# Kernel optimization log

Hardware: AMD Instinct MI355X
Metric: run time of the kernel (lower is better)

## Reference

```python
import jax, jax.numpy as jnp
import numpy as np

N_EMBD = 2048
N_HEAD = 32
N_GROUPS = 8
HEAD_DIM = N_EMBD // N_HEAD
Q_PER_KV = N_HEAD // N_GROUPS
QKV_DIM = (Q_PER_KV + 2) * N_GROUPS * HEAD_DIM


def apply_rope(x, cos, sin):
    # x: [B, nH, T, hd]; cos/sin: [T, rot//2]
    B, nH, T, hd = x.shape
    rot = min(sin.shape[1] * 2, hd)
    half = rot // 2
    x_rot, x_pass = x[..., :rot], x[..., rot:]
    c = cos[:T, :half][None, None]  # [1,1,T,half]
    s = sin[:T, :half][None, None]
    x1, x2 = x_rot[..., :half], x_rot[..., half:]
    x1_ = x1 * c - x2 * s
    x2_ = x2 * c + x1 * s
    return jnp.concatenate([x1_, x2_, x_pass], axis=-1)


def setup_inputs() -> dict:
    key = jax.random.key(0)
    k1, k2, k3, k4, k5 = jax.random.split(key, 5)
    B, T = 2, 2048
    x = jax.random.normal(k1, (B, T, N_EMBD), dtype=jnp.float32)
    cos = jax.random.uniform(k2, (T, HEAD_DIM // 2), dtype=jnp.float32)
    sin = jax.random.uniform(k3, (T, HEAD_DIM // 2), dtype=jnp.float32)
    attn_w = jax.random.normal(k4, (QKV_DIM, N_EMBD), dtype=jnp.float32) * (1.0 / np.sqrt(N_EMBD))
    proj_w = jax.random.normal(k5, (N_EMBD, N_EMBD), dtype=jnp.float32) * (1.0 / np.sqrt(N_EMBD))
    return {"x": x, "cos": cos, "sin": sin, "attn_w": attn_w, "proj_w": proj_w}


def reference(x, cos, sin, attn_w, proj_w):
    B, T, E = x.shape
    qkv = jnp.einsum('bte,fe->btf', x, attn_w)  # [B,T,QKV_DIM]
    qkv = qkv.reshape(B, T, N_GROUPS, Q_PER_KV + 2, HEAD_DIM)
    q = qkv[:, :, :, :Q_PER_KV].reshape(B, T, N_HEAD, HEAD_DIM)
    k = qkv[:, :, :, Q_PER_KV]      # [B,T,G,hd]
    v = qkv[:, :, :, Q_PER_KV + 1]  # [B,T,G,hd]
    # [B, heads, T, hd] layout; GQA repeat_interleave of K/V to full head count
    q = q.transpose(0, 2, 1, 3)
    k = jnp.repeat(k.transpose(0, 2, 1, 3), Q_PER_KV, axis=1)
    v = jnp.repeat(v.transpose(0, 2, 1, 3), Q_PER_KV, axis=1)
    q = apply_rope(q, cos, sin)
    k = apply_rope(k, cos, sin)
    scale = 1.0 / np.sqrt(HEAD_DIM)
    att = jax.nn.softmax(jnp.einsum('bhqd,bhkd->bhqk', q, k) * scale, axis=-1)
    out = jnp.einsum('bhqk,bhkd->bhqd', att, v)  # [B,nH,T,hd]
    out = out.transpose(0, 2, 1, 3).reshape(B, T, N_HEAD * HEAD_DIM)
    return jnp.einsum('bte,fe->btf', out, proj_w)
```

## Files before the change

kernel.cpp:

```cpp
#include <hip/hip_runtime.h>

typedef unsigned short u16;
typedef unsigned int u32;
typedef __bf16 bf16x8 __attribute__((ext_vector_type(8)));
typedef float f32x4 __attribute__((ext_vector_type(4)));
typedef float f32x16 __attribute__((ext_vector_type(16)));

__device__ __forceinline__ u16 f2bf(float f) {
    u32 u = __builtin_bit_cast(u32, f);
    u32 r = u + 0x7FFFu + ((u >> 16) & 1u);
    return (u16)(r >> 16);
}
__device__ __forceinline__ u32 pack_bf16(float v0, float v1) {
    u32 a = __builtin_bit_cast(u32, v0) + 0x8000u;
    u32 b = __builtin_bit_cast(u32, v1) + 0x8000u;
    return __builtin_amdgcn_perm(b, a, 0x07060302u);
}
__device__ __forceinline__ void gload16(const u16* g, u16* l) {
    __builtin_amdgcn_global_load_lds(
        (const __attribute__((address_space(1))) u32*)g,
        (__attribute__((address_space(3))) u32*)l, 16, 0, 0);
}

#define QSCALE 0.18033688011111793f

__global__ __launch_bounds__(256) void cvt_kernel(const float* __restrict__ in,
                                                  u16* __restrict__ out, int n4) {
    int i = blockIdx.x * 256 + threadIdx.x;
    if (i >= n4) return;
    float4 f = reinterpret_cast<const float4*>(in)[i];
    u32 lo = (u32)f2bf(f.x) | ((u32)f2bf(f.y) << 16);
    u32 hi = (u32)f2bf(f.z) | ((u32)f2bf(f.w) << 16);
    reinterpret_cast<uint2*>(out)[i] = make_uint2(lo, hi);
}

__global__ __launch_bounds__(256) void gemm_qkv(const u16* __restrict__ A,
                                                const u16* __restrict__ Bw,
                                                const float* __restrict__ cosb,
                                                const float* __restrict__ sinb,
                                                u16* __restrict__ Qo,
                                                u16* __restrict__ Ko,
                                                u16* __restrict__ Vt) {
    __shared__ __align__(16) u16 As[2 * 128 * 32];
    __shared__ __align__(16) u16 Bs[2 * 128 * 32];
    const int tid = threadIdx.x;
    const int wave = tid >> 6, lane = tid & 63, quad = lane >> 4, l15 = lane & 15;
    const int wm = wave >> 1, wn = wave & 1;
    const int m0 = blockIdx.x * 128, n0 = blockIdx.y * 128;
    const int K = 2048;
    const int lrow = lane >> 2, lcol = (lane & 3) * 8;
    f32x4 acc[4][4];
#pragma unroll
    for (int a = 0; a < 4; a++)
#pragma unroll
        for (int b = 0; b < 4; b++) acc[a][b] = (f32x4){0.f, 0.f, 0.f, 0.f};
    for (int kk = 0; kk < K; kk += 64) {
        __syncthreads();
#pragma unroll
        for (int p = 0; p < 2; p++)
#pragma unroll
            for (int c = 0; c < 2; c++) {
                const int rA = wave * 32 + c * 16;
                gload16(A  + (size_t)(m0 + rA + lrow) * K + kk + p * 32 + lcol,
                        &As[p * 4096 + rA * 32]);
                gload16(Bw + (size_t)(n0 + rA + lrow) * K + kk + p * 32 + lcol,
                        &Bs[p * 4096 + rA * 32]);
            }
        __syncthreads();
#pragma unroll
        for (int p = 0; p < 2; p++) {
            bf16x8 af[4], bfr[4];
#pragma unroll
            for (int t = 0; t < 4; t++) {
                af[t]  = *reinterpret_cast<const bf16x8*>(
                    &As[p * 4096 + (wm * 64 + t * 16 + l15) * 32 + quad * 8]);
                bfr[t] = *reinterpret_cast<const bf16x8*>(
                    &Bs[p * 4096 + (wn * 64 + t * 16 + l15) * 32 + quad * 8]);
            }
#pragma unroll
            for (int tm = 0; tm < 4; tm++)
#pragma unroll
                for (int tn = 0; tn < 4; tn++)
                    acc[tm][tn] = __builtin_amdgcn_mfma_f32_16x16x32_bf16(af[tm], bfr[tn], acc[tm][tn], 0, 0, 0);
        }
    }
    const int slot_base = n0 + wn * 64;
    const int G = slot_base / 384;
    const int slot = (slot_base % 384) / 64;
    const int bb = m0 >> 11;
    const int tb0 = (m0 & 2047) + wm * 64 + quad * 4;
    if (slot == 5) {
        u16* vbase = Vt + ((size_t)(bb * 8 + G) * 64) * 2048;
#pragma unroll
        for (int tm = 0; tm < 4; tm++) {
            const int trow = tb0 + tm * 16;
#pragma unroll
            for (int tn = 0; tn < 4; tn++) {
                const int d = tn * 16 + l15;
                uint2 pk;
                pk.x = pack_bf16(acc[tm][tn][0], acc[tm][tn][1]);
                pk.y = pack_bf16(acc[tm][tn][2], acc[tm][tn][3]);
                *reinterpret_cast<uint2*>(vbase + (size_t)d * 2048 + trow) = pk;
            }
        }
    } else {
        const float sc = (slot < 4) ? QSCALE : 1.0f;
        u16* obase = (slot < 4)
            ? Qo + ((size_t)(bb * 32 + G * 4 + slot) * 2048) * 64
            : Ko + ((size_t)(bb * 8 + G) * 2048) * 64;
#pragma unroll
        for (int tm = 0; tm < 4; tm++) {
#pragma unroll
            for (int i = 0; i < 4; i++) {
                const int t = tb0 + tm * 16 + i;
#pragma unroll
                for (int tn = 0; tn < 2; tn++) {
                    const int dh = tn * 16 + l15;
                    float c = cosb[t * 32 + dh], s = sinb[t * 32 + dh];
                    float x1 = acc[tm][tn][i], x2 = acc[tm][tn + 2][i];
                    obase[(size_t)t * 64 + dh]      = f2bf((x1 * c - x2 * s) * sc);
                    obase[(size_t)t * 64 + dh + 32] = f2bf((x2 * c + x1 * s) * sc);
                }
            }
        }
    }
}

__global__ __launch_bounds__(256) void gemm_bt(const u16* __restrict__ A,
                                               const u16* __restrict__ Bw,
                                               float* __restrict__ Cf,
                                               int M, int N, int K) {
    __shared__ __align__(16) u16 As[2 * 128 * 32];
    __shared__ __align__(16) u16 Bs[2 * 128 * 32];
    const int tid = threadIdx.x;
    const int wave = tid >> 6, lane = tid & 63, quad = lane >> 4, l15 = lane & 15;
    const int wm = wave >> 1, wn = wave & 1;
    const int m0 = blockIdx.x * 128, n0 = blockIdx.y * 128;
    const int lrow = lane >> 2, lcol = (lane & 3) * 8;
    f32x4 acc[4][4];
#pragma unroll
    for (int a = 0; a < 4; a++)
#pragma unroll
        for (int b = 0; b < 4; b++) acc[a][b] = (f32x4){0.f, 0.f, 0.f, 0.f};
    for (int kk = 0; kk < K; kk += 64) {
        __syncthreads();
#pragma unroll
        for (int p = 0; p < 2; p++)
#pragma unroll
            for (int c = 0; c < 2; c++) {
                const int rA = wave * 32 + c * 16;
                gload16(A  + (size_t)(m0 + rA + lrow) * K + kk + p * 32 + lcol,
                        &As[p * 4096 + rA * 32]);
                gload16(Bw + (size_t)(n0 + rA + lrow) * K + kk + p * 32 + lcol,
                        &Bs[p * 4096 + rA * 32]);
            }
        __syncthreads();
#pragma unroll
        for (int p = 0; p < 2; p++) {
            bf16x8 af[4], bfr[4];
#pragma unroll
            for (int t = 0; t < 4; t++) {
                af[t]  = *reinterpret_cast<const bf16x8*>(
                    &As[p * 4096 + (wm * 64 + t * 16 + l15) * 32 + quad * 8]);
                bfr[t] = *reinterpret_cast<const bf16x8*>(
                    &Bs[p * 4096 + (wn * 64 + t * 16 + l15) * 32 + quad * 8]);
            }
#pragma unroll
            for (int tm = 0; tm < 4; tm++)
#pragma unroll
                for (int tn = 0; tn < 4; tn++)
                    acc[tm][tn] = __builtin_amdgcn_mfma_f32_16x16x32_bf16(af[tm], bfr[tn], acc[tm][tn], 0, 0, 0);
        }
    }
#pragma unroll
    for (int tm = 0; tm < 4; tm++) {
        const int r0 = m0 + wm * 64 + tm * 16 + quad * 4;
#pragma unroll
        for (int tn = 0; tn < 4; tn++) {
            const int c = n0 + wn * 64 + tn * 16 + l15;
#pragma unroll
            for (int i = 0; i < 4; i++) Cf[(size_t)(r0 + i) * N + c] = acc[tm][tn][i];
        }
    }
}

__global__ __launch_bounds__(256, 4) void attn(const u16* __restrict__ Q,
                                               const u16* __restrict__ Kg,
                                               const u16* __restrict__ Vt,
                                               u16* __restrict__ O) {
    constexpr int LDK = 72;
    constexpr int LDP = 88;
    __shared__ __align__(16) u16 Ks[64 * LDK];
    __shared__ __align__(16) u16 Vts[64 * LDK];
    __shared__ __align__(16) u16 Ps[4 * 32 * LDP];
    const int tid = threadIdx.x, w = tid >> 6, lane = tid & 63;
    const int half = lane >> 5, l31 = lane & 31;
    const int q0 = blockIdx.x * 128;
    const int h = blockIdx.y, b = blockIdx.z, g = h >> 2;
    const u16* qb = Q + (((size_t)(b * 32 + h)) * 2048 + q0) * 64;
    const u16* kb = Kg + ((size_t)(b * 8 + g)) * 2048 * 64;
    const u16* vb = Vt + ((size_t)(b * 8 + g)) * 64 * 2048;

    {
        const int r = tid >> 3, c = tid & 7;
#pragma unroll
        for (int p = 0; p < 4; p++) {
            uint4 d = *reinterpret_cast<const uint4*>(qb + (size_t)(r + p * 32) * 64 + c * 8);
            *reinterpret_cast<uint4*>(&Ps[(r + p * 32) * LDK + c * 8]) = d;
        }
    }
    __syncthreads();
    bf16x8 qf[4];
#pragma unroll
    for (int ks = 0; ks < 4; ks++)
        qf[ks] = *reinterpret_cast<const bf16x8*>(&Ps[(w * 32 + l31) * LDK + ks * 16 + half * 8]);
    __syncthreads();

    f32x16 Oa[2];
#pragma unroll
    for (int t = 0; t < 2; t++)
#pragma unroll
        for (int i = 0; i < 16; i++) Oa[t][i] = 0.f;
    float lsum = 0.f;
    u16* Pw = Ps + w * 32 * LDP;

    for (int kk = 0; kk < 2048; kk += 64) {
        __syncthreads();
        {
            const int r = tid >> 3, c = tid & 7;
#pragma unroll
            for (int p = 0; p < 2; p++) {
                uint4 dk = *reinterpret_cast<const uint4*>(kb + (size_t)(kk + r + p * 32) * 64 + c * 8);
                *reinterpret_cast<uint4*>(&Ks[(r + p * 32) * LDK + c * 8]) = dk;
                uint4 dv = *reinterpret_cast<const uint4*>(vb + (size_t)(r + p * 32) * 2048 + kk + c * 8);
                *reinterpret_cast<uint4*>(&Vts[(r + p * 32) * LDK + c * 8]) = dv;
            }
        }
        __syncthreads();
        f32x16 S[2];
#pragma unroll
        for (int kt = 0; kt < 2; kt++) {
#pragma unroll
            for (int i = 0; i < 16; i++) S[kt][i] = 0.f;
#pragma unroll
            for (int ks = 0; ks < 4; ks++) {
                bf16x8 kf = *reinterpret_cast<const bf16x8*>(
                    &Ks[(kt * 32 + l31) * LDK + ks * 16 + half * 8]);
                S[kt] = __builtin_amdgcn_mfma_f32_32x32x16_bf16(kf, qf[ks], S[kt], 0, 0, 0);
            }
        }
        float ps = 0.f;
#pragma unroll
        for (int kt = 0; kt < 2; kt++)
#pragma unroll
            for (int gr = 0; gr < 4; gr++) {
                float p0 = __builtin_amdgcn_exp2f(S[kt][gr * 4 + 0]);
                float p1 = __builtin_amdgcn_exp2f(S[kt][gr * 4 + 1]);
                float p2 = __builtin_amdgcn_exp2f(S[kt][gr * 4 + 2]);
                float p3 = __builtin_amdgcn_exp2f(S[kt][gr * 4 + 3]);
                ps += (p0 + p1) + (p2 + p3);
                uint2 pk;
                pk.x = pack_bf16(p0, p1);
                pk.y = pack_bf16(p2, p3);
                *reinterpret_cast<uint2*>(&Pw[l31 * LDP + kt * 32 + gr * 8 + half * 4]) = pk;
            }
        lsum += ps;
#pragma unroll
        for (int ks2 = 0; ks2 < 4; ks2++) {
            bf16x8 pf = *reinterpret_cast<const bf16x8*>(&Pw[l31 * LDP + ks2 * 16 + half * 8]);
#pragma unroll
            for (int dt = 0; dt < 2; dt++) {
                bf16x8 vf = *reinterpret_cast<const bf16x8*>(
                    &Vts[(dt * 32 + l31) * LDK + ks2 * 16 + half * 8]);
                Oa[dt] = __builtin_amdgcn_mfma_f32_32x32x16_bf16(vf, pf, Oa[dt], 0, 0, 0);
            }
        }
    }
    float lt = lsum + __shfl_xor(lsum, 32);
    float linv = 1.f / lt;
    const int t = q0 + w * 32 + l31;
    u16* orow = O + ((size_t)(b * 2048 + t)) * 2048 + h * 64;
#pragma unroll
    for (int dt = 0; dt < 2; dt++)
#pragma unroll
        for (int gr = 0; gr < 4; gr++) {
            uint2 pk;
            pk.x = pack_bf16(Oa[dt][gr * 4 + 0] * linv, Oa[dt][gr * 4 + 1] * linv);
            pk.y = pack_bf16(Oa[dt][gr * 4 + 2] * linv, Oa[dt][gr * 4 + 3] * linv);
            *reinterpret_cast<uint2*>(orow + dt * 32 + 8 * gr + 4 * half) = pk;
        }
}

extern "C" void kernel_launch(void* const* d_in, const int* in_sizes, int n_in,
                              void* d_out, int out_size, void* d_ws, size_t ws_size,
                              hipStream_t stream) {
    const float* x      = (const float*)d_in[0];
    const float* cosb   = (const float*)d_in[1];
    const float* sinb   = (const float*)d_in[2];
    const float* attn_w = (const float*)d_in[3];
    const float* proj_w = (const float*)d_in[4];
    float* out = (float*)d_out;

    u16* xb  = (u16*)d_ws;
    u16* w1b = xb  + (size_t)4096 * 2048;
    u16* w2b = w1b + (size_t)3072 * 2048;
    u16* qo  = w2b + (size_t)2048 * 2048;
    u16* ko  = qo  + (size_t)2 * 32 * 2048 * 64;
    u16* vt  = ko  + (size_t)2 * 8 * 2048 * 64;
    u16* ao  = xb;

    cvt_kernel<<<8192, 256, 0, stream>>>(x, xb, 4096 * 2048 / 4);
    cvt_kernel<<<6144, 256, 0, stream>>>(attn_w, w1b, 3072 * 2048 / 4);
    cvt_kernel<<<4096, 256, 0, stream>>>(proj_w, w2b, 2048 * 2048 / 4);
    gemm_qkv<<<dim3(32, 24), 256, 0, stream>>>(xb, w1b, cosb, sinb, qo, ko, vt);
    attn<<<dim3(16, 32, 2), 256, 0, stream>>>(qo, ko, vt, ao);
    gemm_bt<<<dim3(32, 16), 256, 0, stream>>>(ao, w2b, out, 4096, 2048, 2048);
}
```

Baseline: 338.6 us.

## Double-buffer K/V via async LDS loads and keep P in registers

The attention kernel now stages K/V tiles with global_load_lds into XOR-swizzled, double-buffered shared memory, prefetching the next tile while computing the current one. It also drops the P round-trip through LDS: probabilities are packed with v_cvt_pk_bf16_f32 and rearranged with v_permlane32_swap to form the MFMA B operand in registers. s_setprio is raised around the MFMA blocks. These changes target global-load latency, LDS traffic, bank conflicts and one barrier per iteration, at the cost of more LDS for double buffers, which may reduce occupancy, and reliance on gfx950-specific instructions.

```diff
diff --git a/kernel.cpp b/kernel.cpp
--- a/kernel.cpp
+++ b/kernel.cpp
@@ -5,6 +5,7 @@
 typedef __bf16 bf16x8 __attribute__((ext_vector_type(8)));
 typedef float f32x4 __attribute__((ext_vector_type(4)));
 typedef float f32x16 __attribute__((ext_vector_type(16)));
+typedef unsigned int u32x4 __attribute__((ext_vector_type(4)));
 
 __device__ __forceinline__ u16 f2bf(float f) {
     u32 u = __builtin_bit_cast(u32, f);
@@ -15,6 +16,14 @@
     u32 a = __builtin_bit_cast(u32, v0) + 0x8000u;
     u32 b = __builtin_bit_cast(u32, v1) + 0x8000u;
     return __builtin_amdgcn_perm(b, a, 0x07060302u);
+}
+__device__ __forceinline__ u32 cvtpk(float lo, float hi) {
+    u32 r;
+    asm("v_cvt_pk_bf16_f32 %0, %1, %2" : "=v"(r) : "v"(lo), "v"(hi));
+    return r;
+}
+__device__ __forceinline__ void plswap(u32& a, u32& b) {
+    asm("v_permlane32_swap_b32 %0, %1" : "+v"(a), "+v"(b));
 }
 __device__ __forceinline__ void gload16(const u16* g, u16* l) {
     __builtin_amdgcn_global_load_lds(
@@ -188,32 +197,30 @@
                                                const u16* __restrict__ Kg,
                                                const u16* __restrict__ Vt,
                                                u16* __restrict__ O) {
-    constexpr int LDK = 72;
-    constexpr int LDP = 88;
-    __shared__ __align__(16) u16 Ks[64 * LDK];
-    __shared__ __align__(16) u16 Vts[64 * LDK];
-    __shared__ __align__(16) u16 Ps[4 * 32 * LDP];
+    __shared__ __align__(16) u16 Ks[2 * 64 * 64];
+    __shared__ __align__(16) u16 Vts[2 * 64 * 64];
     const int tid = threadIdx.x, w = tid >> 6, lane = tid & 63;
     const int half = lane >> 5, l31 = lane & 31;
+    const int rsub = lane >> 3;
+    const int csub = (lane & 7) ^ rsub;
+    const int swz = (l31 & 7) << 3;
     const int q0 = blockIdx.x * 128;
     const int h = blockIdx.y, b = blockIdx.z, g = h >> 2;
     const u16* qb = Q + (((size_t)(b * 32 + h)) * 2048 + q0) * 64;
     const u16* kb = Kg + ((size_t)(b * 8 + g)) * 2048 * 64;
     const u16* vb = Vt + ((size_t)(b * 8 + g)) * 64 * 2048;
 
-    {
-        const int r = tid >> 3, c = tid & 7;
-#pragma unroll
-        for (int p = 0; p < 4; p++) {
-            uint4 d = *reinterpret_cast<const uint4*>(qb + (size_t)(r + p * 32) * 64 + c * 8);
-            *reinterpret_cast<uint4*>(&Ps[(r + p * 32) * LDK + c * 8]) = d;
-        }
+#pragma unroll
+    for (int i = 0; i < 4; i++) {
+        const int r = w * 32 + i * 8;
+        gload16(qb + (size_t)(r + rsub) * 64 + csub * 8, Ks + r * 64);
     }
     __syncthreads();
     bf16x8 qf[4];
 #pragma unroll
     for (int ks = 0; ks < 4; ks++)
-        qf[ks] = *reinterpret_cast<const bf16x8*>(&Ps[(w * 32 + l31) * LDK + ks * 16 + half * 8]);
+        qf[ks] = *reinterpret_cast<const bf16x8*>(
+            &Ks[(w * 32 + l31) * 64 + ((ks * 16 + half * 8) ^ swz)]);
     __syncthreads();
 
     f32x16 Oa[2];
@@ -222,59 +229,76 @@
 #pragma unroll
         for (int i = 0; i < 16; i++) Oa[t][i] = 0.f;
     float lsum = 0.f;
-    u16* Pw = Ps + w * 32 * LDP;
-
-    for (int kk = 0; kk < 2048; kk += 64) {
-        __syncthreads();
-        {
-            const int r = tid >> 3, c = tid & 7;
-#pragma unroll
-            for (int p = 0; p < 2; p++) {
-                uint4 dk = *reinterpret_cast<const uint4*>(kb + (size_t)(kk + r + p * 32) * 64 + c * 8);
-                *reinterpret_cast<uint4*>(&Ks[(r + p * 32) * LDK + c * 8]) = dk;
-                uint4 dv = *reinterpret_cast<const uint4*>(vb + (size_t)(r + p * 32) * 2048 + kk + c * 8);
-                *reinterpret_cast<uint4*>(&Vts[(r + p * 32) * LDK + c * 8]) = dv;
-            }
-        }
-        __syncthreads();
-        f32x16 S[2];
+
+    auto stage_kv = [&](int kk, int bsel) {
+        u16* kd = Ks + bsel * 4096;
+        u16* vd = Vts + bsel * 4096;
+        const u16* kg = kb + (size_t)kk * 64;
+        const u16* vg = vb + kk;
+#pragma unroll
+        for (int i = 0; i < 2; i++) {
+            const int r = w * 16 + i * 8;
+            gload16(kg + (size_t)(r + rsub) * 64 + csub * 8, kd + r * 64);
+            gload16(vg + (size_t)(r + rsub) * 2048 + csub * 8, vd + r * 64);
+        }
+    };
+
+    stage_kv(0, 0);
+    __syncthreads();
+
+    for (int t = 0; t < 32; t++) {
+        if (t < 31) stage_kv((t + 1) * 64, (t + 1) & 1);
+        const u16* Kb = Ks + (t & 1) * 4096;
+        const u16* Vb = Vts + (t & 1) * 4096;
+
+        float ps = 0.f;
+        u32 pw[4][4];
 #pragma unroll
         for (int kt = 0; kt < 2; kt++) {
-#pragma unroll
-            for (int i = 0; i < 16; i++) S[kt][i] = 0.f;
+            f32x16 S;
+#pragma unroll
+            for (int i = 0; i < 16; i++) S[i] = 0.f;
+            __builtin_amdgcn_s_setprio(1);
 #pragma unroll
             for (int ks = 0; ks < 4; ks++) {
                 bf16x8 kf = *reinterpret_cast<const bf16x8*>(
-                    &Ks[(kt * 32 + l31) * LDK + ks * 16 + half * 8]);
-                S[kt] = __builtin_amdgcn_mfma_f32_32x32x16_bf16(kf, qf[ks], S[kt], 0, 0, 0);
-            }
-        }
-        float ps = 0.f;
-#pragma unroll
-        for (int kt = 0; kt < 2; kt++)
-#pragma unroll
-            for (int gr = 0; gr < 4; gr++) {
-                float p0 = __builtin_amdgcn_exp2f(S[kt][gr * 4 + 0]);
-                float p1 = __builtin_amdgcn_exp2f(S[kt][gr * 4 + 1]);
-                float p2 = __builtin_amdgcn_exp2f(S[kt][gr * 4 + 2]);
-                float p3 = __builtin_amdgcn_exp2f(S[kt][gr * 4 + 3]);
-                ps += (p0 + p1) + (p2 + p3);
-                uint2 pk;
-                pk.x = pack_bf16(p0, p1);
-                pk.y = pack_bf16(p2, p3);
-                *reinterpret_cast<uint2*>(&Pw[l31 * LDP + kt * 32 + gr * 8 + half * 4]) = pk;
-            }
+                    &Kb[(kt * 32 + l31) * 64 + ((ks * 16 + half * 8) ^ swz)]);
+                S = __builtin_amdgcn_mfma_f32_32x32x16_bf16(kf, qf[ks], S, 0, 0, 0);
+            }
+            __builtin_amdgcn_s_setprio(0);
+            float pe[16];
+#pragma unroll
+            for (int r = 0; r < 16; r++) pe[r] = __builtin_amdgcn_exp2f(S[r]);
+#pragma unroll
+            for (int r = 0; r < 4; r++)
+                ps += (pe[r * 4 + 0] + pe[r * 4 + 1]) + (pe[r * 4 + 2] + pe[r * 4 + 3]);
+#pragma unroll
+            for (int j = 0; j < 2; j++) {
+                u32 X0 = cvtpk(pe[j * 8 + 0], pe[j * 8 + 1]);
+                u32 Y0 = cvtpk(pe[j * 8 + 4], pe[j * 8 + 5]);
+                u32 X1 = cvtpk(pe[j * 8 + 2], pe[j * 8 + 3]);
+                u32 Y1 = cvtpk(pe[j * 8 + 6], pe[j * 8 + 7]);
+                plswap(X0, Y0);
+                plswap(X1, Y1);
+                const int ks2 = kt * 2 + j;
+                pw[ks2][0] = X0; pw[ks2][1] = X1; pw[ks2][2] = Y0; pw[ks2][3] = Y1;
+            }
+        }
         lsum += ps;
+        __builtin_amdgcn_s_setprio(1);
 #pragma unroll
         for (int ks2 = 0; ks2 < 4; ks2++) {
-            bf16x8 pf = *reinterpret_cast<const bf16x8*>(&Pw[l31 * LDP + ks2 * 16 + half * 8]);
+            u32x4 pv = (u32x4){pw[ks2][0], pw[ks2][1], pw[ks2][2], pw[ks2][3]};
+            bf16x8 pf = __builtin_bit_cast(bf16x8, pv);
 #pragma unroll
             for (int dt = 0; dt < 2; dt++) {
                 bf16x8 vf = *reinterpret_cast<const bf16x8*>(
-                    &Vts[(dt * 32 + l31) * LDK + ks2 * 16 + half * 8]);
+                    &Vb[(dt * 32 + l31) * 64 + ((ks2 * 16 + half * 8) ^ swz)]);
                 Oa[dt] = __builtin_amdgcn_mfma_f32_32x32x16_bf16(vf, pf, Oa[dt], 0, 0, 0);
             }
         }
+        __builtin_amdgcn_s_setprio(0);
+        __syncthreads();
     }
     float lt = lsum + __shfl_xor(lsum, 32);
     float linv = 1.f / lt;
```

Measured after the change: 330.2 us. -2.5%, faster.
